# Kernel optimization log

Hardware: AMD Instinct MI355X
Metric: run time of the kernel (lower is better)

The kernel has to match this reference:

```python
import jax, jax.numpy as jnp
import numpy as np

B, C = 2, 4
SPATIAL = (128, 128, 128)
N_PTS = 32          # num_points_per_class
THR = 0.5           # threshold


def setup_inputs() -> dict:
    key = jax.random.key(0)
    logits = jax.random.normal(key, (B, C) + SPATIAL, dtype=jnp.float32)
    return {"logits": logits}


def _extract_points(logits):
    """Vectorized equivalent of the per-(batch,class) nonzero/topk loop.

    For every (b, c): softmax prob > THR defines candidates; top-k by prob
    selects up to N_PTS points. Classes are visited in the original order
    (foreground 1..C-1, then background 0); valid points are compacted to
    the front per batch element; padding has label -1 and coords 0.
    Output width is fixed at C*N_PTS (jit-friendly) instead of the batch
    max count, but all valid (coord, label) entries and their order match.
    """
    b, c = logits.shape[:2]
    spatial = logits.shape[2:]
    dims = len(spatial)
    S = int(np.prod(spatial))
    probs = jax.nn.softmax(logits, axis=1).reshape(b, c, S)  # [b,c,S]
    # class visitation order: 1..C-1 then 0 (background last)
    order = jnp.concatenate([jnp.arange(1, c), jnp.arange(1)])  # [c]
    probs = probs[:, order]                                    # [b,c,S]
    score = jnp.where(probs > THR, probs, -jnp.inf)
    top_vals, top_idx = jax.lax.top_k(score, N_PTS)            # [b,c,N_PTS]
    valid = top_vals > -jnp.inf                                # [b,c,N_PTS]
    coords = jnp.stack(jnp.unravel_index(top_idx, spatial), axis=-1)  # [b,c,N_PTS,dims]
    labels = jnp.where(valid, order[None, :, None], -1)        # [b,c,N_PTS]
    coords = jnp.where(valid[..., None], coords, 0)
    # flatten classes and compact valid points to the front (stable sort)
    N = c * N_PTS
    labels = labels.reshape(b, N)
    coords = coords.reshape(b, N, dims)
    perm = jnp.argsort((labels < 0).astype(jnp.int32), axis=1, stable=True)  # [b,N]
    labels = jnp.take_along_axis(labels, perm, axis=1)
    coords = jnp.take_along_axis(coords, perm[..., None], axis=1)
    return coords.astype(jnp.int32), labels.astype(jnp.int32)


def reference(logits):
    coords, labels = _extract_points(logits)
    return coords, labels
```

## Files before the change

kernel.cpp:

```cpp
#include <hip/hip_runtime.h>
#include <stdint.h>

#define Bn 2
#define Cn 4
#define Sn (128 * 128 * 128)
#define NPTS 32
#define NBINS 1025
#define THRf 0.5f
#define PB 4096
#define BT 512
#define FB 1024

__device__ __forceinline__ int bin_of_bits(unsigned int u) {
    return (int)((u - 0x3F000000u) >> 13);
}

__device__ __forceinline__ void softmax_argmax4(float l0, float l1, float l2, float l3,
                                                int* cm_out, float* p_out) {
    float m = fmaxf(fmaxf(l0, l1), fmaxf(l2, l3));
    float e0 = expf(l0 - m);
    float e1 = expf(l1 - m);
    float e2 = expf(l2 - m);
    float e3 = expf(l3 - m);
    float s = ((e0 + e1) + e2) + e3;
    float em = e0; int cm = 0;
    if (e1 > em) { em = e1; cm = 1; }
    if (e2 > em) { em = e2; cm = 2; }
    if (e3 > em) { em = e3; cm = 3; }
    *cm_out = cm;
    *p_out = em / s;
}

__global__ __launch_bounds__(BT) void fused_kernel(const float* __restrict__ logits,
                                                   unsigned int* __restrict__ cnt,
                                                   unsigned int* __restrict__ gh,
                                                   uint2* __restrict__ cand,
                                                   int cap,
                                                   unsigned int* __restrict__ done,
                                                   unsigned int* __restrict__ done2,
                                                   unsigned int* __restrict__ validn,
                                                   uint2* __restrict__ topk,
                                                   int* __restrict__ out) {
    __shared__ unsigned int lh[Cn * NBINS];
    __shared__ unsigned int lcut[Cn], cls_cnt[Cn], cls_base[Cn], cls_pos[Cn];
    __shared__ unsigned int s_old;
    __shared__ uint2 fbuf[FB];
    __shared__ unsigned int s_T, s_m;
    __shared__ int pre[Cn + 1];

    const int b = blockIdx.y;
    const int t = threadIdx.x;
    const int lane = t & 63;
    for (int j = t; j < Cn * NBINS; j += BT) lh[j] = 0u;
    if (t < Cn) { lcut[t] = 0u; cls_cnt[t] = 0u; cls_pos[t] = 0u; }
    __syncthreads();

    const float* base = logits + (size_t)b * Cn * Sn;
    const float4* s0 = (const float4*)base;
    const float4* s1 = (const float4*)(base + Sn);
    const float4* s2 = (const float4*)(base + 2 * Sn);
    const float4* s3 = (const float4*)(base + 3 * Sn);
    const int qs = blockIdx.x * (PB / 4);
    unsigned int pk[PB / BT];
    #pragma unroll
    for (int it = 0; it < PB / 4 / BT; ++it) {
        int q = qs + it * BT + t;
        float4 v0 = s0[q], v1 = s1[q], v2 = s2[q], v3 = s3[q];
        const float* a0 = &v0.x; const float* a1 = &v1.x;
        const float* a2 = &v2.x; const float* a3 = &v3.x;
        #pragma unroll
        for (int k = 0; k < 4; ++k) {
            int cm; float p;
            softmax_argmax4(a0[k], a1[k], a2[k], a3[k], &cm, &p);
            unsigned int pv = 0u;
            if (p > THRf) {
                unsigned int off = __float_as_uint(p) - 0x3F000000u;
                atomicAdd(&lh[cm * NBINS + (int)(off >> 13)], 1u);
                pv = (off << 2) | (unsigned int)cm;
            }
            pk[it * 4 + k] = pv;
        }
    }
    __syncthreads();

    {
        const int wave = t >> 6;
        if (wave < Cn) {
            const unsigned int* h = &lh[wave * NBINS];
            const int lo = lane * 17;
            unsigned int cs = 0;
            #pragma unroll
            for (int k = 0; k < 17; ++k) {
                int bin = lo + k;
                if (bin < NBINS) cs += h[bin];
            }
            unsigned int S = cs;
            #pragma unroll
            for (int off = 1; off < 64; off <<= 1) {
                unsigned int v = __shfl_down(S, off, 64);
                if (lane + off < 64) S += v;
            }
            unsigned int suf = S - cs;
            if (S >= NPTS && suf < NPTS) {
                unsigned int acc = suf;
                int hi = min(lo + 16, NBINS - 1);
                for (int bin = hi; bin >= lo; --bin) {
                    acc += h[bin];
                    if (acc >= NPTS) {
                        lcut[wave] = (unsigned int)bin;
                        cls_cnt[wave] = acc;
                        break;
                    }
                }
            }
            if (lane == 0 && S < NPTS) cls_cnt[wave] = S;
        }
    }
    __syncthreads();

    {
        const int wave = t >> 6;
        if (wave < Cn) {
            const unsigned int* h = &lh[wave * NBINS];
            unsigned int* g = gh + (size_t)(b * Cn + wave) * NBINS;
            for (int bin = (int)lcut[wave] + lane; bin < NBINS; bin += 64) {
                unsigned int v = h[bin];
                if (v) atomicAdd(&g[bin], v);
            }
        }
    }
    if (t < Cn && cls_cnt[t] > 0)
        cls_base[t] = atomicAdd(&cnt[b * Cn + t], cls_cnt[t]);
    __syncthreads();

    #pragma unroll
    for (int j = 0; j < PB / BT; ++j) {
        unsigned int pv = pk[j];
        if (pv != 0u) {
            unsigned int cm = pv & 3u;
            if ((pv >> 15) >= lcut[cm]) {
                unsigned int pos = cls_base[cm] + atomicAdd(&cls_pos[cm], 1u);
                if (pos < (unsigned int)cap) {
                    int it = j >> 2, k = j & 3;
                    unsigned int idx = (unsigned int)((qs + it * BT + t) * 4 + k);
                    unsigned long long packed =
                        ((unsigned long long)idx << 32) | (0x3F000000u + (pv >> 2));
                    __hip_atomic_store(
                        (unsigned long long*)&cand[(size_t)(b * Cn + cm) * cap + pos],
                        packed, __ATOMIC_RELAXED, __HIP_MEMORY_SCOPE_AGENT);
                }
            }
        }
    }

    __syncthreads();
    if (t == 0) s_old = atomicAdd(&done[b], 1u);
    __syncthreads();
    const unsigned int NX = gridDim.x;
    if (s_old + 4u < NX) return;
    const int csel = (int)(NX - 1u - s_old);
    if (t == 0) {
        while (__hip_atomic_load(&done[b], __ATOMIC_RELAXED, __HIP_MEMORY_SCOPE_AGENT) < NX)
            __builtin_amdgcn_s_sleep(2);
    }
    __syncthreads();
    __threadfence();

    const int bc = b * Cn + csel;
    for (int j = t; j < NBINS; j += BT) lh[j] = gh[(size_t)bc * NBINS + j];
    if (t == 0) { s_T = 0u; s_m = 0u; }
    __syncthreads();
    const int n = min((int)cnt[bc], cap);

    if (t < 64) {
        const int lo = lane * 17;
        unsigned int cs = 0;
        #pragma unroll
        for (int k = 0; k < 17; ++k) {
            int bin = lo + k;
            if (bin < NBINS) cs += lh[bin];
        }
        unsigned int S = cs;
        #pragma unroll
        for (int off = 1; off < 64; off <<= 1) {
            unsigned int v = __shfl_down(S, off, 64);
            if (lane + off < 64) S += v;
        }
        unsigned int suf = S - cs;
        if (S >= NPTS && suf < NPTS) {
            unsigned int acc = suf;
            int hi = min(lo + 16, NBINS - 1);
            for (int bin = hi; bin >= lo; --bin) {
                acc += lh[bin];
                if (acc >= NPTS) { s_T = (unsigned int)bin; break; }
            }
        }
    }
    __syncthreads();
    const unsigned int T = s_T;

    {
        const uint2* src = cand + (size_t)bc * cap;
        for (int j0 = t; j0 < n; j0 += BT * 8) {
            uint2 e[8];
            #pragma unroll
            for (int k = 0; k < 8; ++k) {
                int j = j0 + k * BT;
                e[k] = src[j < n ? j : (n - 1)];
            }
            #pragma unroll
            for (int k = 0; k < 8; ++k) {
                int j = j0 + k * BT;
                if (j < n && (unsigned int)bin_of_bits(e[k].x) >= T) {
                    unsigned int pos = atomicAdd(&s_m, 1u);
                    if (pos < FB) fbuf[pos] = e[k];
                }
            }
        }
    }
    __syncthreads();

    const int m = min((int)s_m, FB);
    const int vn = min(n, NPTS);
    if (t == 0)
        __hip_atomic_store(&validn[bc], (unsigned int)vn,
                           __ATOMIC_RELAXED, __HIP_MEMORY_SCOPE_AGENT);
    for (int i = t; i < m; i += BT) {
        uint2 e = fbuf[i];
        int rank = 0;
        for (int j = 0; j < m; ++j) {
            uint2 o = fbuf[j];
            rank += (int)((o.x > e.x) || (o.x == e.x && o.y < e.y));
        }
        if (rank < vn) {
            unsigned long long packed = ((unsigned long long)e.y << 32) | e.x;
            __hip_atomic_store((unsigned long long*)&topk[bc * NPTS + rank],
                               packed, __ATOMIC_RELAXED, __HIP_MEMORY_SCOPE_AGENT);
        }
    }

    __syncthreads();
    if (t == 0) s_old = atomicAdd(&done2[b], 1u);
    __syncthreads();
    if (s_old != 3u) return;
    __threadfence();

    if (t == 0) {
        int acc = 0;
        for (int oc = 0; oc < Cn; ++oc) {
            pre[oc] = acc;
            acc += (int)validn[b * Cn + ((oc + 1) & 3)];
        }
        pre[Cn] = acc;
    }
    __syncthreads();

    if (t < Cn * NPTS) {
        const int j = t;
        int label = -1, z = 0, y = 0, x = 0;
        if (j < pre[Cn]) {
            int oc = 0;
            while (j >= pre[oc + 1]) ++oc;
            int c = (oc + 1) & 3;
            int r = j - pre[oc];
            uint2 e = topk[(b * Cn + c) * NPTS + r];
            int idx = (int)e.y;
            z = idx >> 14;
            y = (idx >> 7) & 127;
            x = idx & 127;
            label = c;
        }
        int* coords = out;
        int* labels = out + Bn * Cn * NPTS * 3;
        int bo = b * Cn * NPTS + j;
        coords[bo * 3 + 0] = z;
        coords[bo * 3 + 1] = y;
        coords[bo * 3 + 2] = x;
        labels[bo] = label;
    }
}

extern "C" void kernel_launch(void* const* d_in, const int* in_sizes, int n_in,
                              void* d_out, int out_size, void* d_ws, size_t ws_size,
                              hipStream_t stream) {
    const float* logits = (const float*)d_in[0];
    int* out = (int*)d_out;

    unsigned int* cnt = (unsigned int*)d_ws;
    unsigned int* done = cnt + Bn * Cn;
    unsigned int* done2 = done + Bn;
    unsigned int* gh = done2 + Bn;
    unsigned int* validn = gh + Bn * Cn * NBINS;
    uint2* topk = (uint2*)(validn + Bn * Cn);
    uint2* cand = topk + Bn * Cn * NPTS;
    size_t fixed = (size_t)((char*)cand - (char*)d_ws);
    int cap = (int)((ws_size - fixed) / (Bn * Cn * sizeof(uint2)));
    if (cap > (1 << 18)) cap = 1 << 18;
    if (cap < 4096) cap = 4096;

    hipMemsetAsync(cnt, 0,
                   (size_t)(Bn * Cn + Bn + Bn + Bn * Cn * NBINS) * sizeof(unsigned int),
                   stream);

    dim3 grid(Sn / PB, Bn);
    fused_kernel<<<grid, BT, 0, stream>>>(logits, cnt, gh, cand, cap,
                                          done, done2, validn, topk, out);
}
```

Measured before the change: 128.2 us.

## Replace host memset with in-kernel workspace init guarded by a magic flag

Drops the hipMemsetAsync launch and has block 0 of each batch zero the global histogram and counters. A per-batch flag set to a magic value tells other blocks that init is done, and they spin on it before touching global state. The last block clears the flag for the next call. The change also issues all global loads up front before shared-memory init and adds a min-blocks-per-CU launch bound. The risk is that the spin-wait and the reset rely on every block of a batch being resident, and on workspace state left over from the previous call.

```diff
diff --git a/kernel.cpp b/kernel.cpp
--- a/kernel.cpp
+++ b/kernel.cpp
@@ -10,6 +10,7 @@
 #define PB 4096
 #define BT 512
 #define FB 1024
+#define INIT_MAGIC 0x5A17F00Du
 
 __device__ __forceinline__ int bin_of_bits(unsigned int u) {
     return (int)((u - 0x3F000000u) >> 13);
@@ -31,16 +32,17 @@
     *p_out = em / s;
 }
 
-__global__ __launch_bounds__(BT) void fused_kernel(const float* __restrict__ logits,
-                                                   unsigned int* __restrict__ cnt,
-                                                   unsigned int* __restrict__ gh,
-                                                   uint2* __restrict__ cand,
-                                                   int cap,
-                                                   unsigned int* __restrict__ done,
-                                                   unsigned int* __restrict__ done2,
-                                                   unsigned int* __restrict__ validn,
-                                                   uint2* __restrict__ topk,
-                                                   int* __restrict__ out) {
+__global__ __launch_bounds__(BT, 8) void fused_kernel(const float* __restrict__ logits,
+                                                      unsigned int* __restrict__ cnt,
+                                                      unsigned int* __restrict__ gh,
+                                                      uint2* __restrict__ cand,
+                                                      int cap,
+                                                      unsigned int* __restrict__ done,
+                                                      unsigned int* __restrict__ done2,
+                                                      unsigned int* __restrict__ iflag,
+                                                      unsigned int* __restrict__ validn,
+                                                      uint2* __restrict__ topk,
+                                                      int* __restrict__ out) {
     __shared__ unsigned int lh[Cn * NBINS];
     __shared__ unsigned int lcut[Cn], cls_cnt[Cn], cls_base[Cn], cls_pos[Cn];
     __shared__ unsigned int s_old;
@@ -51,9 +53,6 @@
     const int b = blockIdx.y;
     const int t = threadIdx.x;
     const int lane = t & 63;
-    for (int j = t; j < Cn * NBINS; j += BT) lh[j] = 0u;
-    if (t < Cn) { lcut[t] = 0u; cls_cnt[t] = 0u; cls_pos[t] = 0u; }
-    __syncthreads();
 
     const float* base = logits + (size_t)b * Cn * Sn;
     const float4* s0 = (const float4*)base;
@@ -61,26 +60,50 @@
     const float4* s2 = (const float4*)(base + 2 * Sn);
     const float4* s3 = (const float4*)(base + 3 * Sn);
     const int qs = blockIdx.x * (PB / 4);
+    const int q0 = qs + t;
+    const int q1 = qs + BT + t;
+    float4 u0 = s0[q0], u1 = s1[q0], u2 = s2[q0], u3 = s3[q0];
+    float4 w0 = s0[q1], w1 = s1[q1], w2 = s2[q1], w3 = s3[q1];
+
+    if (blockIdx.x == 0) {
+        unsigned int* gz = gh + (size_t)b * Cn * NBINS;
+        for (int j = t; j < Cn * NBINS; j += BT)
+            __hip_atomic_store(&gz[j], 0u, __ATOMIC_RELAXED, __HIP_MEMORY_SCOPE_AGENT);
+        if (t < Cn)
+            __hip_atomic_store(&cnt[b * Cn + t], 0u, __ATOMIC_RELAXED, __HIP_MEMORY_SCOPE_AGENT);
+        if (t == Cn)
+            __hip_atomic_store(&done[b], 0u, __ATOMIC_RELAXED, __HIP_MEMORY_SCOPE_AGENT);
+        if (t == Cn + 1)
+            __hip_atomic_store(&done2[b], 0u, __ATOMIC_RELAXED, __HIP_MEMORY_SCOPE_AGENT);
+        __syncthreads();
+        if (t == 0)
+            __hip_atomic_store(&iflag[b], INIT_MAGIC, __ATOMIC_RELAXED, __HIP_MEMORY_SCOPE_AGENT);
+    }
+
+    for (int j = t; j < Cn * NBINS; j += BT) lh[j] = 0u;
+    if (t < Cn) { lcut[t] = 0u; cls_cnt[t] = 0u; cls_pos[t] = 0u; }
+    __syncthreads();
+
     unsigned int pk[PB / BT];
-    #pragma unroll
-    for (int it = 0; it < PB / 4 / BT; ++it) {
-        int q = qs + it * BT + t;
-        float4 v0 = s0[q], v1 = s1[q], v2 = s2[q], v3 = s3[q];
-        const float* a0 = &v0.x; const float* a1 = &v1.x;
-        const float* a2 = &v2.x; const float* a3 = &v3.x;
-        #pragma unroll
-        for (int k = 0; k < 4; ++k) {
-            int cm; float p;
-            softmax_argmax4(a0[k], a1[k], a2[k], a3[k], &cm, &p);
-            unsigned int pv = 0u;
-            if (p > THRf) {
-                unsigned int off = __float_as_uint(p) - 0x3F000000u;
-                atomicAdd(&lh[cm * NBINS + (int)(off >> 13)], 1u);
-                pv = (off << 2) | (unsigned int)cm;
-            }
-            pk[it * 4 + k] = pv;
-        }
-    }
+    #define PROC4(V0, V1, V2, V3, IT) do {                                        \
+        const float* a0 = &V0.x; const float* a1 = &V1.x;                         \
+        const float* a2 = &V2.x; const float* a3 = &V3.x;                         \
+        _Pragma("unroll")                                                         \
+        for (int k = 0; k < 4; ++k) {                                             \
+            int cm; float p;                                                      \
+            softmax_argmax4(a0[k], a1[k], a2[k], a3[k], &cm, &p);                 \
+            unsigned int pv = 0u;                                                 \
+            if (p > THRf) {                                                       \
+                unsigned int off = __float_as_uint(p) - 0x3F000000u;              \
+                atomicAdd(&lh[cm * NBINS + (int)(off >> 13)], 1u);                \
+                pv = (off << 2) | (unsigned int)cm;                               \
+            }                                                                     \
+            pk[(IT) * 4 + k] = pv;                                                \
+        }                                                                         \
+    } while (0)
+    PROC4(u0, u1, u2, u3, 0);
+    PROC4(w0, w1, w2, w3, 1);
+    #undef PROC4
     __syncthreads();
 
     {
@@ -115,6 +138,13 @@
             }
             if (lane == 0 && S < NPTS) cls_cnt[wave] = S;
         }
+    }
+    __syncthreads();
+
+    if (t == 0) {
+        while (__hip_atomic_load(&iflag[b], __ATOMIC_RELAXED, __HIP_MEMORY_SCOPE_AGENT)
+               != INIT_MAGIC)
+            __builtin_amdgcn_s_sleep(2);
     }
     __syncthreads();
 
@@ -278,6 +308,9 @@
         coords[bo * 3 + 2] = x;
         labels[bo] = label;
     }
+    __syncthreads();
+    if (t == 0)
+        __hip_atomic_store(&iflag[b], 0u, __ATOMIC_RELAXED, __HIP_MEMORY_SCOPE_AGENT);
 }
 
 extern "C" void kernel_launch(void* const* d_in, const int* in_sizes, int n_in,
@@ -289,20 +322,17 @@
     unsigned int* cnt = (unsigned int*)d_ws;
     unsigned int* done = cnt + Bn * Cn;
     unsigned int* done2 = done + Bn;
-    unsigned int* gh = done2 + Bn;
+    unsigned int* iflag = done2 + Bn;
+    unsigned int* gh = iflag + Bn;
     unsigned int* validn = gh + Bn * Cn * NBINS;
-    uint2* topk = (uint2*)(validn + Bn * Cn);
+    uint2* topk = (uint2*)(validn + Bn * Cn + 2);
     uint2* cand = topk + Bn * Cn * NPTS;
     size_t fixed = (size_t)((char*)cand - (char*)d_ws);
     int cap = (int)((ws_size - fixed) / (Bn * Cn * sizeof(uint2)));
     if (cap > (1 << 18)) cap = 1 << 18;
     if (cap < 4096) cap = 4096;
 
-    hipMemsetAsync(cnt, 0,
-                   (size_t)(Bn * Cn + Bn + Bn + Bn * Cn * NBINS) * sizeof(unsigned int),
-                   stream);
-
     dim3 grid(Sn / PB, Bn);
     fused_kernel<<<grid, BT, 0, stream>>>(logits, cnt, gh, cand, cap,
-                                          done, done2, validn, topk, out);
+                                          done, done2, iflag, validn, topk, out);
 }
```

Result: slower. 159.2 us (+24.2%).

## Split fused kernel into stream pass and separate select/emit kernel

Applied to the files above, without the earlier changes.

Replaces the single persistent-style kernel, whose last four blocks per batch spin-waited on a global done counter before doing selection, with two launches. The first launch streams logits, builds the histograms and writes candidates with plain stores. A second 8-block kernel of 1024 threads does the threshold search, the ranking and the output emission. This removes the spin-wait and the atomic stores, and widens the selection blocks. In exchange it adds a kernel launch boundary and a second memset-free handoff through global memory.

```diff
diff --git a/kernel.cpp b/kernel.cpp
--- a/kernel.cpp
+++ b/kernel.cpp
@@ -9,6 +9,7 @@
 #define THRf 0.5f
 #define PB 4096
 #define BT 512
+#define BT2 1024
 #define FB 1024
 
 __device__ __forceinline__ int bin_of_bits(unsigned int u) {
@@ -31,23 +32,14 @@
     *p_out = em / s;
 }
 
-__global__ __launch_bounds__(BT) void fused_kernel(const float* __restrict__ logits,
+
+__global__ __launch_bounds__(BT) void fused_stream(const float* __restrict__ logits,
                                                    unsigned int* __restrict__ cnt,
                                                    unsigned int* __restrict__ gh,
                                                    uint2* __restrict__ cand,
-                                                   int cap,
-                                                   unsigned int* __restrict__ done,
-                                                   unsigned int* __restrict__ done2,
-                                                   unsigned int* __restrict__ validn,
-                                                   uint2* __restrict__ topk,
-                                                   int* __restrict__ out) {
+                                                   int cap) {
     __shared__ unsigned int lh[Cn * NBINS];
     __shared__ unsigned int lcut[Cn], cls_cnt[Cn], cls_base[Cn], cls_pos[Cn];
-    __shared__ unsigned int s_old;
-    __shared__ uint2 fbuf[FB];
-    __shared__ unsigned int s_T, s_m;
-    __shared__ int pre[Cn + 1];
-
     const int b = blockIdx.y;
     const int t = threadIdx.x;
     const int lane = t & 63;
@@ -143,31 +135,31 @@
                 if (pos < (unsigned int)cap) {
                     int it = j >> 2, k = j & 3;
                     unsigned int idx = (unsigned int)((qs + it * BT + t) * 4 + k);
-                    unsigned long long packed =
-                        ((unsigned long long)idx << 32) | (0x3F000000u + (pv >> 2));
-                    __hip_atomic_store(
-                        (unsigned long long*)&cand[(size_t)(b * Cn + cm) * cap + pos],
-                        packed, __ATOMIC_RELAXED, __HIP_MEMORY_SCOPE_AGENT);
+                    cand[(size_t)(b * Cn + cm) * cap + pos] =
+                        make_uint2(0x3F000000u + (pv >> 2), idx);
                 }
             }
         }
     }
-
-    __syncthreads();
-    if (t == 0) s_old = atomicAdd(&done[b], 1u);
-    __syncthreads();
-    const unsigned int NX = gridDim.x;
-    if (s_old + 4u < NX) return;
-    const int csel = (int)(NX - 1u - s_old);
-    if (t == 0) {
-        while (__hip_atomic_load(&done[b], __ATOMIC_RELAXED, __HIP_MEMORY_SCOPE_AGENT) < NX)
-            __builtin_amdgcn_s_sleep(2);
-    }
-    __syncthreads();
-    __threadfence();
-
-    const int bc = b * Cn + csel;
-    for (int j = t; j < NBINS; j += BT) lh[j] = gh[(size_t)bc * NBINS + j];
+}
+
+__global__ __launch_bounds__(BT2) void select_emit(const unsigned int* __restrict__ cnt,
+                                                   const unsigned int* __restrict__ gh,
+                                                   const uint2* __restrict__ cand,
+                                                   int cap,
+                                                   unsigned int* __restrict__ done,
+                                                   unsigned int* __restrict__ validn,
+                                                   uint2* __restrict__ topk,
+                                                   int* __restrict__ out) {
+    __shared__ unsigned int lh[NBINS];
+    __shared__ uint2 fbuf[FB];
+    __shared__ unsigned int s_T, s_m, s_old;
+    __shared__ int pre[Cn + 1];
+    const int bc = blockIdx.x, t = threadIdx.x;
+    const int b = bc >> 2;
+    const int lane = t & 63;
+
+    for (int j = t; j < NBINS; j += BT2) lh[j] = gh[(size_t)bc * NBINS + j];
     if (t == 0) { s_T = 0u; s_m = 0u; }
     __syncthreads();
     const int n = min((int)cnt[bc], cap);
@@ -201,16 +193,16 @@
 
     {
         const uint2* src = cand + (size_t)bc * cap;
-        for (int j0 = t; j0 < n; j0 += BT * 8) {
+        for (int j0 = t; j0 < n; j0 += BT2 * 8) {
             uint2 e[8];
             #pragma unroll
             for (int k = 0; k < 8; ++k) {
-                int j = j0 + k * BT;
-                e[k] = src[j < n ? j : (n - 1)];
+                int j = j0 + k * BT2;
+                e[k] = src[j < n ? j : (n > 0 ? n - 1 : 0)];
             }
             #pragma unroll
             for (int k = 0; k < 8; ++k) {
-                int j = j0 + k * BT;
+                int j = j0 + k * BT2;
                 if (j < n && (unsigned int)bin_of_bits(e[k].x) >= T) {
                     unsigned int pos = atomicAdd(&s_m, 1u);
                     if (pos < FB) fbuf[pos] = e[k];
@@ -222,25 +214,20 @@
 
     const int m = min((int)s_m, FB);
     const int vn = min(n, NPTS);
-    if (t == 0)
-        __hip_atomic_store(&validn[bc], (unsigned int)vn,
-                           __ATOMIC_RELAXED, __HIP_MEMORY_SCOPE_AGENT);
-    for (int i = t; i < m; i += BT) {
+    if (t == 0) validn[bc] = (unsigned int)vn;
+    for (int i = t; i < m; i += BT2) {
         uint2 e = fbuf[i];
         int rank = 0;
         for (int j = 0; j < m; ++j) {
             uint2 o = fbuf[j];
             rank += (int)((o.x > e.x) || (o.x == e.x && o.y < e.y));
         }
-        if (rank < vn) {
-            unsigned long long packed = ((unsigned long long)e.y << 32) | e.x;
-            __hip_atomic_store((unsigned long long*)&topk[bc * NPTS + rank],
-                               packed, __ATOMIC_RELAXED, __HIP_MEMORY_SCOPE_AGENT);
-        }
-    }
-
-    __syncthreads();
-    if (t == 0) s_old = atomicAdd(&done2[b], 1u);
+        if (rank < vn) topk[bc * NPTS + rank] = e;
+    }
+
+    __threadfence();
+    __syncthreads();
+    if (t == 0) s_old = atomicAdd(&done[b], 1u);
     __syncthreads();
     if (s_old != 3u) return;
     __threadfence();
@@ -288,8 +275,7 @@
 
     unsigned int* cnt = (unsigned int*)d_ws;
     unsigned int* done = cnt + Bn * Cn;
-    unsigned int* done2 = done + Bn;
-    unsigned int* gh = done2 + Bn;
+    unsigned int* gh = done + Bn;
     unsigned int* validn = gh + Bn * Cn * NBINS;
     uint2* topk = (uint2*)(validn + Bn * Cn);
     uint2* cand = topk + Bn * Cn * NPTS;
@@ -298,11 +284,10 @@
     if (cap > (1 << 18)) cap = 1 << 18;
     if (cap < 4096) cap = 4096;
 
-    hipMemsetAsync(cnt, 0,
-                   (size_t)(Bn * Cn + Bn + Bn + Bn * Cn * NBINS) * sizeof(unsigned int),
+    hipMemsetAsync(cnt, 0, (size_t)(Bn * Cn + Bn + Bn * Cn * NBINS) * sizeof(unsigned int),
                    stream);
 
     dim3 grid(Sn / PB, Bn);
-    fused_kernel<<<grid, BT, 0, stream>>>(logits, cnt, gh, cand, cap,
-                                          done, done2, validn, topk, out);
-}
+    fused_stream<<<grid, BT, 0, stream>>>(logits, cnt, gh, cand, cap);
+    select_emit<<<Bn * Cn, BT2, 0, stream>>>(cnt, gh, cand, cap, done, validn, topk, out);
+}
```

New measurement: 117.8 us. 1.09x faster.
